# Optimization experiments

Measured on AMD Instinct MI355X. Metric: run time of the kernel, lower is better.

The kernel has to match this reference:

```python
import jax, jax.numpy as jnp
import numpy as np

B, T, E = 2, 2048, 2048
H, HKV, D = 32, 8, 64
G = H // HKV  # groups = 4
ROPE_BASE = 10000.0


def setup_inputs() -> dict:
    key = jax.random.key(0)
    ks = jax.random.split(key, 5)
    s = 0.02
    return {
        "x": jax.random.normal(ks[0], (B, T, E), dtype=jnp.float32),
        "Wq": jax.random.normal(ks[1], (E, H * D), dtype=jnp.float32) * s,
        "Wk": jax.random.normal(ks[2], (E, HKV * D), dtype=jnp.float32) * s,
        "Wv": jax.random.normal(ks[3], (E, HKV * D), dtype=jnp.float32) * s,
        "Wo": jax.random.normal(ks[4], (E, E), dtype=jnp.float32) * s,
    }


def _rope_tables(t, d, dtype):
    # standard rotate-half RoPE, theta base 10000
    inv_freq = 1.0 / (ROPE_BASE ** (jnp.arange(0, d, 2, dtype=jnp.float32) / d))
    ang = jnp.arange(t, dtype=jnp.float32)[:, None] * inv_freq[None, :]  # [T, D/2]
    return jnp.cos(ang).astype(dtype), jnp.sin(ang).astype(dtype)


def _apply_rope(x, cos, sin):
    # x: [B, h, T, D]; cos/sin: [T, D/2]
    d2 = x.shape[-1] // 2
    x1, x2 = x[..., :d2], x[..., d2:]
    return jnp.concatenate([x1 * cos - x2 * sin, x2 * cos + x1 * sin], axis=-1)


def reference(x, Wq, Wk, Wv, Wo):
    b, t, _ = x.shape
    q = (x @ Wq).reshape(b, t, H, D).transpose(0, 2, 1, 3)      # [B,H,T,D]
    k = (x @ Wk).reshape(b, t, HKV, D).transpose(0, 2, 1, 3)    # [B,HKV,T,D]
    v = (x @ Wv).reshape(b, t, HKV, D).transpose(0, 2, 1, 3)    # [B,HKV,T,D]

    cos, sin = _rope_tables(t, D, x.dtype)
    q = _apply_rope(q, cos, sin)
    k = _apply_rope(k, cos, sin)

    # GQA: keep KV unexpanded, broadcast groups inside the contraction
    qg = q.reshape(b, HKV, G, t, D)
    scale = 1.0 / np.sqrt(D)
    scores = jnp.einsum('bkgtd,bksd->bkgts', qg, k) * scale      # [B,HKV,G,T,T]
    causal = jnp.tril(jnp.ones((t, t), dtype=bool))
    scores = jnp.where(causal, scores, jnp.finfo(scores.dtype).min)
    attn = jax.nn.softmax(scores, axis=-1)
    y = jnp.einsum('bkgts,bksd->bkgtd', attn, v)                 # [B,HKV,G,T,D]
    y = y.reshape(b, H, t, D).transpose(0, 2, 1, 3).reshape(b, t, H * D)
    return y @ Wo
```

## Files before the change

kernel.cpp:

```cpp
#include <hip/hip_runtime.h>
#include <hip/hip_bf16.h>
#include <cstdint>
#include <cstddef>

typedef __bf16 bf16;
typedef __attribute__((ext_vector_type(8))) __bf16 bf16x8;
typedef __attribute__((ext_vector_type(4))) __bf16 bf16x4v;
typedef __attribute__((ext_vector_type(4))) float f32x4;

#define NB 2
#define NT 2048
#define NE 2048
#define NH 32
#define NHKV 8
#define ND 64
#define NBT (NB * NT)
#define NQKV 3072

__device__ __forceinline__ void gload_lds16(const void* g, void* l) {
  __builtin_amdgcn_global_load_lds(
      (const __attribute__((address_space(1))) unsigned int*)g,
      (__attribute__((address_space(3))) unsigned int*)l, 16, 0, 0);
}

__device__ __forceinline__ int swz(int row, int byteoff) {
  return (row * 128 + byteoff) ^ ((row & 7) << 4);
}


__global__ __launch_bounds__(256)
void prep_kernel(const float* __restrict__ x, const float* __restrict__ Wq,
                 const float* __restrict__ Wk, const float* __restrict__ Wv,
                 const float* __restrict__ Wo, bf16* __restrict__ xb,
                 bf16* __restrict__ wqkv_t, bf16* __restrict__ wo_t,
                 float* __restrict__ tab) {
  const int bid = blockIdx.x, tid = threadIdx.x;

  if (bid < 1024) {
    const int n4 = NBT * NE / 4;
    for (int i = bid * 256 + tid; i < n4; i += 1024 * 256) {
      const float4 v = ((const float4*)x)[i];
      bf16x4v o;
      o[0] = (bf16)v.x; o[1] = (bf16)v.y; o[2] = (bf16)v.z; o[3] = (bf16)v.w;
      ((bf16x4v*)xb)[i] = o;
    }
    return;
  }
  if (bid < 1280) {
    const int i = (bid - 1024) * 256 + tid;
    const int t = i >> 5, d = i & 31;
    const float inv = expf(-(float)d * 0.28782313662425574f);
    const float ang = (float)t * inv;
    tab[t * 64 + d] = cosf(ang);
    tab[t * 64 + 32 + d] = sinf(ang);
    return;
  }

  __shared__ float tile[32][33];
  const float* in;
  bf16* outp;
  int ncols, rowoff, gx, sub;
  if (bid < 5376)      { sub = bid - 1280; in = Wq; outp = wqkv_t; ncols = 2048; rowoff = 0;    gx = 64; }
  else if (bid < 6400) { sub = bid - 5376; in = Wk; outp = wqkv_t; ncols = 512;  rowoff = 2048; gx = 16; }
  else if (bid < 7424) { sub = bid - 6400; in = Wv; outp = wqkv_t; ncols = 512;  rowoff = 2560; gx = 16; }
  else                 { sub = bid - 7424; in = Wo; outp = wo_t;   ncols = 2048; rowoff = 0;    gx = 64; }
  const int c0 = (sub % gx) * 32, k0 = (sub / gx) * 32;
  const int tx = tid & 31, ty = tid >> 5;
#pragma unroll
  for (int j = 0; j < 4; ++j)
    tile[ty + j * 8][tx] = in[(size_t)(k0 + ty + j * 8) * ncols + c0 + tx];
  __syncthreads();
#pragma unroll
  for (int j = 0; j < 4; ++j)
    outp[(size_t)(rowoff + c0 + ty + j * 8) * 2048 + k0 + tx] = (bf16)tile[tx][ty + j * 8];
}


template <typename CT, bool ROPE>
__global__ __launch_bounds__(256, 3)
void gemm_r3_kernel(const bf16* __restrict__ A, const bf16* __restrict__ Bt,
                    CT* __restrict__ C, int M, int N, int K,
                    const float* __restrict__ tab, bf16* __restrict__ vt) {
  __shared__ __align__(16) bf16 As[3][128 * 32];
  __shared__ __align__(16) bf16 Bs[3][128 * 32];
  const int tid = threadIdx.x;
  const int lane = tid & 63, wid = tid >> 6;
  const int wr = wid >> 1, wc = wid & 1;
  const int cpx = (int)gridDim.x >> 3;
  const int swzb = ((int)blockIdx.x & 7) * cpx + ((int)blockIdx.x >> 3);
  const int gx = N >> 7;
  const int bx = swzb % gx, by = swzb / gx;
  const int m0 = by * 128, n0 = bx * 128;
  const int srow = tid >> 2;
  const int skoff = 8 * ((tid & 3) ^ ((tid >> 3) & 3));
  const bf16* ga = A + (size_t)(m0 + srow) * K + skoff;
  const bf16* gb = Bt + (size_t)(n0 + srow) * K + skoff;
  const int fr = lane & 15;
  const int fq = lane >> 4;
  const int fks = 8 * (fq ^ ((fr >> 1) & 3));
  const int NTK = K >> 5;
  f32x4 acc[4][4] = {};

#define STAGE_T(b, t)                                                   \
  do {                                                                  \
    const int kk = (t) * 32;                                            \
    gload_lds16(ga + kk, &As[b][tid * 8]);                              \
    gload_lds16(ga + kk + (size_t)64 * K, &As[b][2048 + tid * 8]);      \
    gload_lds16(gb + kk, &Bs[b][tid * 8]);                              \
    gload_lds16(gb + kk + (size_t)64 * K, &Bs[b][2048 + tid * 8]);      \
  } while (0)

  STAGE_T(0, 0);
  STAGE_T(1, 1);

  int bc = 0;
  for (int t = 0; t < NTK; ++t) {
    if (t + 1 < NTK) asm volatile("s_waitcnt vmcnt(4)" ::: "memory");
    else             asm volatile("s_waitcnt vmcnt(0)" ::: "memory");
    __builtin_amdgcn_s_barrier();

    bf16x8 af[4], bfr[4];
#pragma unroll
    for (int m = 0; m < 4; ++m)
      af[m] = *(const bf16x8*)&As[bc][(wr * 64 + m * 16 + fr) * 32 + fks];
#pragma unroll
    for (int n = 0; n < 4; ++n)
      bfr[n] = *(const bf16x8*)&Bs[bc][(wc * 64 + n * 16 + fr) * 32 + fks];

    if (t + 2 < NTK) {
      const int pb = (bc + 2 >= 3) ? bc - 1 : bc + 2;
      STAGE_T(pb, t + 2);
    }

    __builtin_amdgcn_s_setprio(1);
#pragma unroll
    for (int m = 0; m < 4; ++m)
#pragma unroll
      for (int n = 0; n < 4; ++n)
        acc[m][n] = __builtin_amdgcn_mfma_f32_16x16x32_bf16(af[m], bfr[n], acc[m][n], 0, 0, 0);
    __builtin_amdgcn_s_setprio(0);
    bc = (bc + 1 == 3) ? 0 : bc + 1;
  }
#undef STAGE_T

  const int colbase = n0 + wc * 64;

  if (ROPE && colbase >= 2560) {
    const int hk = (colbase - 2560) >> 6;
    const int bb = m0 >> 11;
    const int t0 = (m0 & (NT - 1)) + wr * 64 + fq * 4;
    bf16* vtp = vt + (size_t)(bb * NHKV + hk) * 64 * NT;
#pragma unroll
    for (int m = 0; m < 4; ++m) {
#pragma unroll
      for (int n = 0; n < 4; ++n) {
        const int d = n * 16 + fr;
        bf16x4v w;
        w[0] = (bf16)acc[m][n][0];
        w[1] = (bf16)acc[m][n][1];
        w[2] = (bf16)acc[m][n][2];
        w[3] = (bf16)acc[m][n][3];
        *(bf16x4v*)&vtp[(size_t)d * NT + t0 + m * 16] = w;
      }
    }
    return;
  }

  const bool do_rope = ROPE && colbase < 2560;
  const bool do_scale = ROPE && colbase < 2048;
  const float SCALE = 0.18033688011112042f;
  const int orow0 = m0 + wr * 64 + fq * 4;
  const int ocol0 = colbase + fr;
#pragma unroll
  for (int m = 0; m < 4; ++m) {
#pragma unroll
    for (int j = 0; j < 4; ++j) {
      const int row = orow0 + m * 16 + j;
      float v0 = acc[m][0][j], v1 = acc[m][1][j], v2 = acc[m][2][j], v3 = acc[m][3][j];
      if (do_rope) {
        const int tt = row & (NT - 1);
        const float c0 = tab[tt * 64 + fr],      s0 = tab[tt * 64 + 32 + fr];
        const float c1 = tab[tt * 64 + 16 + fr], s1 = tab[tt * 64 + 48 + fr];
        const float a0 = v0, a2 = v2;
        v0 = a0 * c0 - a2 * s0;
        v2 = a2 * c0 + a0 * s0;
        const float a1 = v1, a3 = v3;
        v1 = a1 * c1 - a3 * s1;
        v3 = a3 * c1 + a1 * s1;
        if (do_scale) { v0 *= SCALE; v1 *= SCALE; v2 *= SCALE; v3 *= SCALE; }
      }
      CT* cp = &C[(size_t)row * N + ocol0];
      cp[0] = (CT)v0; cp[16] = (CT)v1; cp[32] = (CT)v2; cp[48] = (CT)v3;
    }
  }
}


__global__ __launch_bounds__(256, 3)
void attn_kernel(const bf16* __restrict__ qkv, const bf16* __restrict__ vt,
                 bf16* __restrict__ y) {
  const int bid = blockIdx.x;
  const int qtb = 15 - (bid >> 6);
  const int bh = bid & 63;
  const int b = bh >> 5, h = bh & 31, hk = h >> 2;
  const int q0 = qtb * 128;

  __shared__ __align__(16) bf16 Kb[2][4096], Vb[2][4096];

  const int tid = threadIdx.x;
  const int lane = tid & 63, wid = tid >> 6;
  const int ql = lane & 15;
  const int sub = lane >> 4;

  const int st_r = tid >> 3;
  const int kperm = 4 * (st_r >> 4) + 8 * ((st_r >> 2) & 3) + (st_r & 3);
  const int csw = ((tid & 7) ^ (st_r & 7)) * 8;
  const bf16* kgbase = qkv + (size_t)(b * NT + kperm) * NQKV + 2048 + hk * 64 + csw;
  const bf16* vgbase = vt + ((size_t)(b * NHKV + hk) * 64 + st_r) * NT + csw;

  auto STAGE = [&](int buf, int kv0) {
    const bf16* kg = kgbase + (size_t)kv0 * NQKV;
    gload_lds16(kg, Kb[buf] + tid * 8);
    gload_lds16(kg + (size_t)32 * NQKV, Kb[buf] + 2048 + tid * 8);
    const bf16* vg = vgbase + kv0;
    gload_lds16(vg, Vb[buf] + tid * 8);
    gload_lds16(vg + 32 * NT, Vb[buf] + 2048 + tid * 8);
  };

  bf16x8 qf[2][2];
#pragma unroll
  for (int set = 0; set < 2; ++set) {
    const bf16* qp = qkv + (size_t)(b * NT + q0 + wid * 32 + set * 16 + ql) * NQKV + h * 64 + sub * 8;
    qf[set][0] = *(const bf16x8*)qp;
    qf[set][1] = *(const bf16x8*)(qp + 32);
  }

  bf16x8 ones8;
#pragma unroll
  for (int i = 0; i < 8; ++i) ones8[i] = (bf16)1.0f;

  f32x4 o[2][4] = {};
  f32x4 ol[2] = {};
  float m_s[2] = {-1e30f, -1e30f};

  const int ntiles = 2 * qtb + 2;
  STAGE(0, 0);

  for (int it = 0; it < ntiles; ++it) {
    const int kv0 = it * 64;
    const int bc = it & 1;
    asm volatile("s_waitcnt vmcnt(0)" ::: "memory");
    __builtin_amdgcn_s_barrier();
    if (it + 1 < ntiles) STAGE(bc ^ 1, kv0 + 64);

    if (kv0 <= q0 + wid * 32 + 47) {
      bf16x8 kf[4][2];
#pragma unroll
      for (int n = 0; n < 4; ++n)
#pragma unroll
        for (int c = 0; c < 2; ++c)
          kf[n][c] = *(const bf16x8*)((const char*)Kb[bc] + swz(n * 16 + ql, c * 64 + sub * 16));
      bf16x8 vf[2][4];
#pragma unroll
      for (int kc = 0; kc < 2; ++kc)
#pragma unroll
        for (int dt = 0; dt < 4; ++dt)
          vf[kc][dt] = *(const bf16x8*)((const char*)Vb[bc] + swz(dt * 16 + ql, kc * 64 + sub * 16));

#pragma unroll
      for (int set = 0; set < 2; ++set) {
        const int qlo = q0 + wid * 32 + set * 16;
        if (kv0 > qlo + 15) continue;

        f32x4 s[4] = {};
        __builtin_amdgcn_s_setprio(1);
#pragma unroll
        for (int n = 0; n < 4; ++n) {
          s[n] = __builtin_amdgcn_mfma_f32_16x16x32_bf16(kf[n][0], qf[set][0], s[n], 0, 0, 0);
          s[n] = __builtin_amdgcn_mfma_f32_16x16x32_bf16(kf[n][1], qf[set][1], s[n], 0, 0, 0);
        }
        __builtin_amdgcn_s_setprio(0);

        float p[4][4];
        if (kv0 + 63 > qlo) {
          const int qrow = qlo + ql;
#pragma unroll
          for (int n = 0; n < 4; ++n) {
            const int kvb = kv0 + 32 * (n >> 1) + 4 * (n & 1) + 8 * sub;
#pragma unroll
            for (int j = 0; j < 4; ++j)
              p[n][j] = (kvb + j > qrow) ? -1e30f : s[n][j];
          }
        } else {
#pragma unroll
          for (int n = 0; n < 4; ++n)
#pragma unroll
            for (int j = 0; j < 4; ++j)
              p[n][j] = s[n][j];
        }

        float rmax = p[0][0];
#pragma unroll
        for (int n = 0; n < 4; ++n)
#pragma unroll
          for (int j = 0; j < 4; ++j) rmax = fmaxf(rmax, p[n][j]);
        rmax = fmaxf(rmax, __shfl_xor(rmax, 16));
        rmax = fmaxf(rmax, __shfl_xor(rmax, 32));

        if (!__all(rmax <= m_s[set] + 8.0f)) {
          const float mnew = fmaxf(m_s[set], rmax);
          const float sc = exp2f(m_s[set] - mnew);
          m_s[set] = mnew;
          ol[set] *= sc;
#pragma unroll
          for (int dt = 0; dt < 4; ++dt) o[set][dt] *= sc;
        }
        const float mcur = m_s[set];

        bf16x8 pb2[2];
#pragma unroll
        for (int n = 0; n < 4; ++n)
#pragma unroll
          for (int j = 0; j < 4; ++j)
            pb2[n >> 1][(n & 1) * 4 + j] = (bf16)exp2f(p[n][j] - mcur);

        __builtin_amdgcn_s_setprio(1);
#pragma unroll
        for (int kc = 0; kc < 2; ++kc) {
          ol[set] = __builtin_amdgcn_mfma_f32_16x16x32_bf16(ones8, pb2[kc], ol[set], 0, 0, 0);
#pragma unroll
          for (int dt = 0; dt < 4; ++dt)
            o[set][dt] = __builtin_amdgcn_mfma_f32_16x16x32_bf16(vf[kc][dt], pb2[kc], o[set][dt], 0, 0, 0);
        }
        __builtin_amdgcn_s_setprio(0);
      }
    }
  }

#pragma unroll
  for (int set = 0; set < 2; ++set) {
    const float inv = 1.0f / ol[set][0];
    bf16* yp = y + (size_t)(b * NT + q0 + wid * 32 + set * 16 + ql) * NE + h * 64 + sub * 4;
#pragma unroll
    for (int dt = 0; dt < 4; ++dt) {
      bf16x4v w;
      w[0] = (bf16)(o[set][dt][0] * inv);
      w[1] = (bf16)(o[set][dt][1] * inv);
      w[2] = (bf16)(o[set][dt][2] * inv);
      w[3] = (bf16)(o[set][dt][3] * inv);
      *(bf16x4v*)(yp + dt * 16) = w;
    }
  }
}


extern "C" void kernel_launch(void* const* d_in, const int* in_sizes, int n_in,
                              void* d_out, int out_size, void* d_ws, size_t ws_size,
                              hipStream_t stream) {
  const float* x = (const float*)d_in[0];
  const float* Wq = (const float*)d_in[1];
  const float* Wk = (const float*)d_in[2];
  const float* Wv = (const float*)d_in[3];
  const float* Wo = (const float*)d_in[4];
  float* out = (float*)d_out;

  char* ws = (char*)d_ws;
  size_t off = 0;
  auto alloc = [&](size_t bytes) -> void* {
    void* p = ws + off;
    off += (bytes + 255) & ~(size_t)255;
    return p;
  };
  bf16* xb = (bf16*)alloc((size_t)NBT * NE * 2);
  bf16* wqkv_t = (bf16*)alloc((size_t)NQKV * NE * 2);
  bf16* wo_t = (bf16*)alloc((size_t)NE * NE * 2);
  bf16* qkv = (bf16*)alloc((size_t)NBT * NQKV * 2);
  bf16* vtb = (bf16*)alloc((size_t)NB * NHKV * ND * NT * 2);
  bf16* yb = (bf16*)alloc((size_t)NBT * NE * 2);
  float* tab = (float*)alloc((size_t)NT * 64 * 4);

  prep_kernel<<<11520, 256, 0, stream>>>(x, Wq, Wk, Wv, Wo, xb, wqkv_t, wo_t, tab);
  gemm_r3_kernel<bf16, true><<<dim3((NQKV / 128) * (NBT / 128)), 256, 0, stream>>>(
      xb, wqkv_t, qkv, NBT, NQKV, NE, tab, vtb);
  attn_kernel<<<dim3(NT / 128 * 64), 256, 0, stream>>>(qkv, vtb, yb);
  gemm_r3_kernel<float, false><<<dim3((NE / 128) * (NBT / 128)), 256, 0, stream>>>(
      yb, wo_t, out, NBT, NE, NE, nullptr, nullptr);
}
```

Before: 190.9 us.

## Pair complementary 64-row query tiles per block for balanced causal attention work

Each attention block now processes two 64-row query tiles, one near the start and one near the end of the sequence (pidx and 31-pidx), running exactly 33 KV tiles per block instead of a variable count. This evens out causal-attention work across blocks and removes the long-tail imbalance of the largest-first 128-row schedule. The trade-off is that each wave now handles one 16-row set instead of two, so K/V tiles loaded into LDS are reused by half as many query rows. That roughly doubles total LDS staging traffic for the same compute.

```diff
diff --git a/kernel.cpp b/kernel.cpp
--- a/kernel.cpp
+++ b/kernel.cpp
@@ -200,10 +200,12 @@
 void attn_kernel(const bf16* __restrict__ qkv, const bf16* __restrict__ vt,
                  bf16* __restrict__ y) {
   const int bid = blockIdx.x;
-  const int qtb = 15 - (bid >> 6);
+  const int pidx = bid >> 6;
   const int bh = bid & 63;
   const int b = bh >> 5, h = bh & 31, hk = h >> 2;
-  const int q0 = qtb * 128;
+  const int q0A = pidx * 64;
+  const int q0B = (31 - pidx) * 64;
+  const int ntA = pidx + 1;
 
   __shared__ __align__(16) bf16 Kb[2][4096], Vb[2][4096];
 
@@ -227,130 +229,142 @@
     gload_lds16(vg + 32 * NT, Vb[buf] + 2048 + tid * 8);
   };
 
-  bf16x8 qf[2][2];
-#pragma unroll
-  for (int set = 0; set < 2; ++set) {
-    const bf16* qp = qkv + (size_t)(b * NT + q0 + wid * 32 + set * 16 + ql) * NQKV + h * 64 + sub * 8;
-    qf[set][0] = *(const bf16x8*)qp;
-    qf[set][1] = *(const bf16x8*)(qp + 32);
+  bf16x8 qfA[2], qfB[2];
+  {
+    const bf16* qp = qkv + (size_t)(b * NT + q0A + wid * 16 + ql) * NQKV + h * 64 + sub * 8;
+    qfA[0] = *(const bf16x8*)qp;
+    qfA[1] = *(const bf16x8*)(qp + 32);
+    const bf16* qp2 = qkv + (size_t)(b * NT + q0B + wid * 16 + ql) * NQKV + h * 64 + sub * 8;
+    qfB[0] = *(const bf16x8*)qp2;
+    qfB[1] = *(const bf16x8*)(qp2 + 32);
   }
 
   bf16x8 ones8;
 #pragma unroll
   for (int i = 0; i < 8; ++i) ones8[i] = (bf16)1.0f;
 
-  f32x4 o[2][4] = {};
-  f32x4 ol[2] = {};
-  float m_s[2] = {-1e30f, -1e30f};
-
-  const int ntiles = 2 * qtb + 2;
+  f32x4 o[4] = {};
+  f32x4 ol = {};
+  float m_s = -1e30f;
+
+  auto FLUSH = [&](int q0) {
+    const float inv = 1.0f / ol[0];
+    bf16* yp = y + (size_t)(b * NT + q0 + wid * 16 + ql) * NE + h * 64 + sub * 4;
+#pragma unroll
+    for (int dt = 0; dt < 4; ++dt) {
+      bf16x4v w;
+      w[0] = (bf16)(o[dt][0] * inv);
+      w[1] = (bf16)(o[dt][1] * inv);
+      w[2] = (bf16)(o[dt][2] * inv);
+      w[3] = (bf16)(o[dt][3] * inv);
+      *(bf16x4v*)(yp + dt * 16) = w;
+    }
+  };
+
   STAGE(0, 0);
 
-  for (int it = 0; it < ntiles; ++it) {
-    const int kv0 = it * 64;
-    const int bc = it & 1;
+  for (int f = 0; f < 33; ++f) {
+    const bool phB = (f >= ntA);
+    const int kv0 = (phB ? f - ntA : f) * 64;
+    const int bc = f & 1;
     asm volatile("s_waitcnt vmcnt(0)" ::: "memory");
     __builtin_amdgcn_s_barrier();
-    if (it + 1 < ntiles) STAGE(bc ^ 1, kv0 + 64);
-
-    if (kv0 <= q0 + wid * 32 + 47) {
-      bf16x8 kf[4][2];
+    if (f + 1 < 33) {
+      const int nf = f + 1;
+      const int nkv = (nf >= ntA ? nf - ntA : nf) * 64;
+      STAGE(bc ^ 1, nkv);
+    }
+
+    const int qlo = (phB ? q0B : q0A) + wid * 16;
+
+    bf16x8 kf[4][2];
+#pragma unroll
+    for (int n = 0; n < 4; ++n)
+#pragma unroll
+      for (int c = 0; c < 2; ++c)
+        kf[n][c] = *(const bf16x8*)((const char*)Kb[bc] + swz(n * 16 + ql, c * 64 + sub * 16));
+    bf16x8 vf[2][4];
+#pragma unroll
+    for (int kc = 0; kc < 2; ++kc)
+#pragma unroll
+      for (int dt = 0; dt < 4; ++dt)
+        vf[kc][dt] = *(const bf16x8*)((const char*)Vb[bc] + swz(dt * 16 + ql, kc * 64 + sub * 16));
+
+    const bf16x8 qf0 = phB ? qfB[0] : qfA[0];
+    const bf16x8 qf1 = phB ? qfB[1] : qfA[1];
+
+    f32x4 s[4] = {};
+    __builtin_amdgcn_s_setprio(1);
+#pragma unroll
+    for (int n = 0; n < 4; ++n) {
+      s[n] = __builtin_amdgcn_mfma_f32_16x16x32_bf16(kf[n][0], qf0, s[n], 0, 0, 0);
+      s[n] = __builtin_amdgcn_mfma_f32_16x16x32_bf16(kf[n][1], qf1, s[n], 0, 0, 0);
+    }
+    __builtin_amdgcn_s_setprio(0);
+
+    float p[4][4];
+    if (kv0 + 63 > qlo) {
+      const int qrow = qlo + ql;
+#pragma unroll
+      for (int n = 0; n < 4; ++n) {
+        const int kvb = kv0 + 32 * (n >> 1) + 4 * (n & 1) + 8 * sub;
+#pragma unroll
+        for (int j = 0; j < 4; ++j)
+          p[n][j] = (kvb + j > qrow) ? -1e30f : s[n][j];
+      }
+    } else {
 #pragma unroll
       for (int n = 0; n < 4; ++n)
 #pragma unroll
-        for (int c = 0; c < 2; ++c)
-          kf[n][c] = *(const bf16x8*)((const char*)Kb[bc] + swz(n * 16 + ql, c * 64 + sub * 16));
-      bf16x8 vf[2][4];
-#pragma unroll
-      for (int kc = 0; kc < 2; ++kc)
-#pragma unroll
-        for (int dt = 0; dt < 4; ++dt)
-          vf[kc][dt] = *(const bf16x8*)((const char*)Vb[bc] + swz(dt * 16 + ql, kc * 64 + sub * 16));
-
-#pragma unroll
-      for (int set = 0; set < 2; ++set) {
-        const int qlo = q0 + wid * 32 + set * 16;
-        if (kv0 > qlo + 15) continue;
-
-        f32x4 s[4] = {};
-        __builtin_amdgcn_s_setprio(1);
-#pragma unroll
-        for (int n = 0; n < 4; ++n) {
-          s[n] = __builtin_amdgcn_mfma_f32_16x16x32_bf16(kf[n][0], qf[set][0], s[n], 0, 0, 0);
-          s[n] = __builtin_amdgcn_mfma_f32_16x16x32_bf16(kf[n][1], qf[set][1], s[n], 0, 0, 0);
-        }
-        __builtin_amdgcn_s_setprio(0);
-
-        float p[4][4];
-        if (kv0 + 63 > qlo) {
-          const int qrow = qlo + ql;
-#pragma unroll
-          for (int n = 0; n < 4; ++n) {
-            const int kvb = kv0 + 32 * (n >> 1) + 4 * (n & 1) + 8 * sub;
-#pragma unroll
-            for (int j = 0; j < 4; ++j)
-              p[n][j] = (kvb + j > qrow) ? -1e30f : s[n][j];
-          }
-        } else {
-#pragma unroll
-          for (int n = 0; n < 4; ++n)
-#pragma unroll
-            for (int j = 0; j < 4; ++j)
-              p[n][j] = s[n][j];
-        }
-
-        float rmax = p[0][0];
-#pragma unroll
-        for (int n = 0; n < 4; ++n)
-#pragma unroll
-          for (int j = 0; j < 4; ++j) rmax = fmaxf(rmax, p[n][j]);
-        rmax = fmaxf(rmax, __shfl_xor(rmax, 16));
-        rmax = fmaxf(rmax, __shfl_xor(rmax, 32));
-
-        if (!__all(rmax <= m_s[set] + 8.0f)) {
-          const float mnew = fmaxf(m_s[set], rmax);
-          const float sc = exp2f(m_s[set] - mnew);
-          m_s[set] = mnew;
-          ol[set] *= sc;
-#pragma unroll
-          for (int dt = 0; dt < 4; ++dt) o[set][dt] *= sc;
-        }
-        const float mcur = m_s[set];
-
-        bf16x8 pb2[2];
-#pragma unroll
-        for (int n = 0; n < 4; ++n)
-#pragma unroll
-          for (int j = 0; j < 4; ++j)
-            pb2[n >> 1][(n & 1) * 4 + j] = (bf16)exp2f(p[n][j] - mcur);
-
-        __builtin_amdgcn_s_setprio(1);
-#pragma unroll
-        for (int kc = 0; kc < 2; ++kc) {
-          ol[set] = __builtin_amdgcn_mfma_f32_16x16x32_bf16(ones8, pb2[kc], ol[set], 0, 0, 0);
-#pragma unroll
-          for (int dt = 0; dt < 4; ++dt)
-            o[set][dt] = __builtin_amdgcn_mfma_f32_16x16x32_bf16(vf[kc][dt], pb2[kc], o[set][dt], 0, 0, 0);
-        }
-        __builtin_amdgcn_s_setprio(0);
-      }
-    }
-  }
-
-#pragma unroll
-  for (int set = 0; set < 2; ++set) {
-    const float inv = 1.0f / ol[set][0];
-    bf16* yp = y + (size_t)(b * NT + q0 + wid * 32 + set * 16 + ql) * NE + h * 64 + sub * 4;
-#pragma unroll
-    for (int dt = 0; dt < 4; ++dt) {
-      bf16x4v w;
-      w[0] = (bf16)(o[set][dt][0] * inv);
-      w[1] = (bf16)(o[set][dt][1] * inv);
-      w[2] = (bf16)(o[set][dt][2] * inv);
-      w[3] = (bf16)(o[set][dt][3] * inv);
-      *(bf16x4v*)(yp + dt * 16) = w;
-    }
-  }
+        for (int j = 0; j < 4; ++j)
+          p[n][j] = s[n][j];
+    }
+
+    float rmax = p[0][0];
+#pragma unroll
+    for (int n = 0; n < 4; ++n)
+#pragma unroll
+      for (int j = 0; j < 4; ++j) rmax = fmaxf(rmax, p[n][j]);
+    rmax = fmaxf(rmax, __shfl_xor(rmax, 16));
+    rmax = fmaxf(rmax, __shfl_xor(rmax, 32));
+
+    if (!__all(rmax <= m_s + 8.0f)) {
+      const float mnew = fmaxf(m_s, rmax);
+      const float sc = exp2f(m_s - mnew);
+      m_s = mnew;
+      ol *= sc;
+#pragma unroll
+      for (int dt = 0; dt < 4; ++dt) o[dt] *= sc;
+    }
+    const float mcur = m_s;
+
+    bf16x8 pb2[2];
+#pragma unroll
+    for (int n = 0; n < 4; ++n)
+#pragma unroll
+      for (int j = 0; j < 4; ++j)
+        pb2[n >> 1][(n & 1) * 4 + j] = (bf16)exp2f(p[n][j] - mcur);
+
+    __builtin_amdgcn_s_setprio(1);
+#pragma unroll
+    for (int kc = 0; kc < 2; ++kc) {
+      ol = __builtin_amdgcn_mfma_f32_16x16x32_bf16(ones8, pb2[kc], ol, 0, 0, 0);
+#pragma unroll
+      for (int dt = 0; dt < 4; ++dt)
+        o[dt] = __builtin_amdgcn_mfma_f32_16x16x32_bf16(vf[kc][dt], pb2[kc], o[dt], 0, 0, 0);
+    }
+    __builtin_amdgcn_s_setprio(0);
+
+    if (f == ntA - 1) {
+      FLUSH(q0A);
+#pragma unroll
+      for (int dt = 0; dt < 4; ++dt) o[dt] = f32x4{};
+      ol = f32x4{};
+      m_s = -1e30f;
+    }
+  }
+
+  FLUSH(q0B);
 }
 
 
@@ -382,7 +396,7 @@
   prep_kernel<<<11520, 256, 0, stream>>>(x, Wq, Wk, Wv, Wo, xb, wqkv_t, wo_t, tab);
   gemm_r3_kernel<bf16, true><<<dim3((NQKV / 128) * (NBT / 128)), 256, 0, stream>>>(
       xb, wqkv_t, qkv, NBT, NQKV, NE, tab, vtb);
-  attn_kernel<<<dim3(NT / 128 * 64), 256, 0, stream>>>(qkv, vtb, yb);
+  attn_kernel<<<dim3(16 * 64), 256, 0, stream>>>(qkv, vtb, yb);
   gemm_r3_kernel<float, false><<<dim3((NE / 128) * (NBT / 128)), 256, 0, stream>>>(
       yb, wo_t, out, NBT, NE, NE, nullptr, nullptr);
 }
```

New measurement: 208.5 us. +9.2%, slower.
